# Performance work log

Hardware: AMD Instinct MI355X
Metric: run time of the kernel (lower is better)

## Reference

```python
import jax, jax.numpy as jnp
import numpy as np
import math

# Model dims (from init_kwargs + mamba_ssm Mamba2 defaults)
D_MODEL = 1024
EXPAND = 2
HEADDIM = 64
D_STATE = 64
D_CONV = 4
NGROUPS = 1
D_INNER = EXPAND * D_MODEL            # 2048
NHEADS = D_INNER // HEADDIM           # 32
CONV_DIM = D_INNER + 2 * NGROUPS * D_STATE   # 2176
D_IN_PROJ = 2 * D_INNER + 2 * NGROUPS * D_STATE + NHEADS  # 4256
BATCH, SEQLEN = 4, 2048
RMS_EPS = 1.1920929e-07   # torch.finfo(float32).eps (nn.RMSNorm eps=None)
GNORM_EPS = 1e-5          # mamba_ssm RMSNormGated eps


def _rmsnorm(x, w, eps):
    return x * jax.lax.rsqrt(jnp.mean(x * x, axis=-1, keepdims=True) + eps) * w


def setup_inputs() -> dict:
    key = jax.random.key(0)
    ks = jax.random.split(key, 8)
    x = jax.random.normal(ks[0], (BATCH, SEQLEN, D_MODEL), jnp.float32)
    # router MLP (Linear(d_model,32) -> SiLU -> Linear(32,3))
    r_w1 = jax.random.normal(ks[1], (32, D_MODEL), jnp.float32) / math.sqrt(D_MODEL)
    r_b1 = jnp.zeros((32,), jnp.float32)
    r_w2 = jax.random.normal(ks[2], (3, 32), jnp.float32) / math.sqrt(32)
    r_b2 = jnp.zeros((3,), jnp.float32)
    # Mamba2 params
    in_proj_w = jax.random.normal(ks[3], (D_IN_PROJ, D_MODEL), jnp.float32) / math.sqrt(D_MODEL)
    conv_w = jax.random.normal(ks[4], (CONV_DIM, D_CONV), jnp.float32) * 0.2
    conv_b = jnp.zeros((CONV_DIM,), jnp.float32)
    dt_bias = jax.random.normal(ks[5], (NHEADS,), jnp.float32) * 0.1
    # OrthoSSM multi-scale override: A_log[i] = log(0.001 * 2**i)
    A_log = jnp.log(0.001 * (2.0 ** jnp.arange(NHEADS, dtype=jnp.float32)))
    D_param = jnp.ones((NHEADS,), jnp.float32)
    gnorm_w = jnp.ones((D_INNER,), jnp.float32)
    out_proj_w = jax.random.normal(ks[6], (D_MODEL, D_INNER), jnp.float32) / math.sqrt(D_INNER)
    norm_w = jnp.ones((D_MODEL,), jnp.float32)
    return {"x": x, "norm_w": norm_w, "r_w1": r_w1, "r_b1": r_b1, "r_w2": r_w2,
            "r_b2": r_b2, "in_proj_w": in_proj_w, "conv_w": conv_w, "conv_b": conv_b,
            "dt_bias": dt_bias, "A_log": A_log, "D_param": D_param,
            "gnorm_w": gnorm_w, "out_proj_w": out_proj_w}


def _forward(x, norm_w, r_w1, r_b1, r_w2, r_b2, in_proj_w, conv_w, conv_b,
             dt_bias, A_log, D_param, gnorm_w, out_proj_w):
    B, S, Dm = x.shape
    x_norm = _rmsnorm(x, norm_w, RMS_EPS)
    # --- router: mean-pool -> tiny MLP -> softmax over 3 tiers ---
    h = jax.nn.silu(x_norm.mean(axis=1) @ r_w1.T + r_b1)
    probs = jax.nn.softmax(h @ r_w2.T + r_b2, axis=-1)   # [B,3]
    p_fast = probs[:, 0][:, None, None]
    p_mamba = (probs[:, 1] + probs[:, 2])[:, None, None]
    # --- Mamba2(x_norm) ---
    zxbcdt = x_norm @ in_proj_w.T                         # [B,S,4256]
    z, xBC, dt = jnp.split(zxbcdt, [D_INNER, D_INNER + CONV_DIM], axis=-1)
    # causal depthwise conv1d (kernel 4) + SiLU
    conv = jax.lax.conv_general_dilated(
        xBC.transpose(0, 2, 1), conv_w[:, None, :], (1,), [(D_CONV - 1, 0)],
        feature_group_count=CONV_DIM)                      # [B,CONV_DIM,S]
    xBC = jax.nn.silu(conv.transpose(0, 2, 1) + conv_b)    # [B,S,CONV_DIM]
    xh, Bmat, Cmat = jnp.split(xBC, [D_INNER, D_INNER + NGROUPS * D_STATE], axis=-1)
    xh = xh.reshape(B, S, NHEADS, HEADDIM)                 # [B,S,H,P]
    dt = jax.nn.softplus(dt + dt_bias)                     # [B,S,H]
    A = -jnp.exp(A_log)                                    # [H]
    dA = jnp.exp(dt * A)                                   # [B,S,H]

    def step(hstate, inp):
        dA_t, dt_t, x_t, B_t, C_t = inp
        # hstate: [B,H,P,N]
        hstate = hstate * dA_t[..., None, None] \
                 + (dt_t[..., None] * x_t)[..., None] * B_t[:, None, None, :]
        y_t = jnp.einsum('bhpn,bn->bhp', hstate, C_t)
        return hstate, y_t

    h0 = jnp.zeros((B, NHEADS, HEADDIM, D_STATE), x.dtype)
    xs = (dA.transpose(1, 0, 2), dt.transpose(1, 0, 2), xh.transpose(1, 0, 2, 3),
          Bmat.transpose(1, 0, 2), Cmat.transpose(1, 0, 2))
    _, ys = jax.lax.scan(step, h0, xs)                     # [S,B,H,P]
    y = ys.transpose(1, 0, 2, 3) + D_param[:, None] * xh   # D skip connection
    y = y.reshape(B, S, D_INNER)
    # gated RMSNorm: norm(y * silu(z)) * weight
    yg = y * jax.nn.silu(z)
    yg = _rmsnorm(yg, gnorm_w, GNORM_EPS)
    mamba_out = yg @ out_proj_w.T                          # [B,S,D]
    out = p_fast * x_norm + p_mamba * mamba_out
    return x + out


def reference(x, norm_w, r_w1, r_b1, r_w2, r_b2, in_proj_w, conv_w, conv_b,
              dt_bias, A_log, D_param, gnorm_w, out_proj_w):
    return _forward(x, norm_w, r_w1, r_b1, r_w2, r_b2, in_proj_w, conv_w, conv_b,
                    dt_bias, A_log, D_param, gnorm_w, out_proj_w)
```

## Files before the change

kernel.cpp:

```cpp
#include <hip/hip_runtime.h>
#include <math.h>

typedef __bf16 bf16;
typedef __bf16 bf16x8 __attribute__((ext_vector_type(8)));
typedef __bf16 bf16x4 __attribute__((ext_vector_type(4)));
typedef float f32x4 __attribute__((ext_vector_type(4)));

#define DEV static __device__ __forceinline__
#define AS1 __attribute__((address_space(1)))
#define AS3 __attribute__((address_space(3)))

constexpr int kBatch = 4, kSeq = 2048, kDModel = 1024;
constexpr int kDInner = 2048, kHeads = 32;
constexpr int kConvDim = 2176, kDInProj = 4256, kNPad1 = 4352;
constexpr int kRows = kBatch * kSeq;
constexpr int kChunk = 64, kNChunk = kSeq / kChunk;
constexpr float kRmsEps = 1.1920929e-07f;
constexpr float kGnEps = 1e-5f;

DEV float siluf(float x) { return x / (1.f + expf(-x)); }

DEV float block_reduce_sum(float v, float* red, int tid) {
#pragma unroll
  for (int m = 1; m < 64; m <<= 1) v += __shfl_xor(v, m);
  if ((tid & 63) == 0) red[tid >> 6] = v;
  __syncthreads();
  return red[0] + red[1] + red[2] + red[3];
}

__global__ __launch_bounds__(256) void k_rmsnorm(const float* __restrict__ x,
                                                 const float* __restrict__ nw,
                                                 bf16* __restrict__ xnb) {
  const int row = blockIdx.x;
  const int tid = threadIdx.x;
  float4 v = ((const float4*)(x + (size_t)row * kDModel))[tid];
  __shared__ float red[4];
  float ss = block_reduce_sum(v.x * v.x + v.y * v.y + v.z * v.z + v.w * v.w, red, tid);
  float scale = rsqrtf(ss * (1.f / kDModel) + kRmsEps);
  float4 wv = ((const float4*)nw)[tid];
  bf16x4 ov;
  ov[0] = (bf16)(v.x * scale * wv.x);
  ov[1] = (bf16)(v.y * scale * wv.y);
  ov[2] = (bf16)(v.z * scale * wv.z);
  ov[3] = (bf16)(v.w * scale * wv.w);
  *(bf16x4*)(xnb + (size_t)row * kDModel + tid * 4) = ov;
}

__global__ __launch_bounds__(128) void k_pool1(const bf16* __restrict__ xnb,
                                               float* __restrict__ part) {
  const int g = blockIdx.x, b = blockIdx.y;
  const int tid = threadIdx.x;
  const bf16* base = xnb + ((size_t)b * kSeq + (size_t)g * 32) * kDModel + tid * 8;
  float acc[8] = {0, 0, 0, 0, 0, 0, 0, 0};
  for (int r = 0; r < 32; ++r) {
    bf16x8 v = *(const bf16x8*)(base + (size_t)r * kDModel);
#pragma unroll
    for (int j = 0; j < 8; ++j) acc[j] += (float)v[j];
  }
  float* o = part + ((size_t)b * 64 + g) * kDModel + tid * 8;
#pragma unroll
  for (int j = 0; j < 8; ++j) o[j] = acc[j];
}

__global__ __launch_bounds__(256) void k_pool2(const float* __restrict__ part,
                                               float* __restrict__ mean) {
  const int idx = blockIdx.x * 256 + threadIdx.x;
  const int b = idx >> 10, d = idx & 1023;
  float s = 0.f;
  for (int g = 0; g < 64; ++g) s += part[((size_t)b * 64 + g) * kDModel + d];
  mean[idx] = s * (1.f / kSeq);
}

__global__ __launch_bounds__(128) void k_router(const float* __restrict__ mean,
                                                const float* __restrict__ w1,
                                                const float* __restrict__ b1,
                                                const float* __restrict__ w2,
                                                const float* __restrict__ b2,
                                                float* __restrict__ pfm) {
  __shared__ float hbuf[4][32];
  __shared__ float logit[4][3];
  const int t = threadIdx.x;
  {
    int b = t >> 5, j = t & 31;
    float s = b1[j];
    for (int d = 0; d < kDModel; ++d) s += mean[b * kDModel + d] * w1[j * kDModel + d];
    hbuf[b][j] = siluf(s);
  }
  __syncthreads();
  if (t < 12) {
    int b = t / 3, k = t % 3;
    float s = b2[k];
    for (int j = 0; j < 32; ++j) s += hbuf[b][j] * w2[k * 32 + j];
    logit[b][k] = s;
  }
  __syncthreads();
  if (t < 4) {
    float m = fmaxf(logit[t][0], fmaxf(logit[t][1], logit[t][2]));
    float e0 = expf(logit[t][0] - m), e1 = expf(logit[t][1] - m), e2 = expf(logit[t][2] - m);
    float inv = 1.f / (e0 + e1 + e2);
    pfm[t] = e0 * inv;
    pfm[4 + t] = (e1 + e2) * inv;
  }
}

__global__ __launch_bounds__(256) void k_castpad_w1(const float* __restrict__ w,
                                                    bf16* __restrict__ wb) {
  const size_t idx = (size_t)blockIdx.x * 256 + threadIdx.x;
  const int row = (int)(idx >> 10);
  wb[idx] = (bf16)(row < kDInProj ? w[idx] : 0.f);
}

__global__ __launch_bounds__(256) void k_cast_w2(const float* __restrict__ w,
                                                 bf16* __restrict__ wb) {
  const size_t i4 = (size_t)blockIdx.x * 256 + threadIdx.x;
  float4 v = ((const float4*)w)[i4];
  bf16x4 o;
  o[0] = (bf16)v.x; o[1] = (bf16)v.y; o[2] = (bf16)v.z; o[3] = (bf16)v.w;
  ((bf16x4*)wb)[i4] = o;
}

template <int MF>
__global__ __launch_bounds__(512, 2) void k_gemm(
    const bf16* __restrict__ A, const bf16* __restrict__ B,
    bf16* __restrict__ Cb, float* __restrict__ Cf,
    int K, int Nreal, int ldc, int ntn, int outBf16) {
  constexpr int BM = MF * 32;
  constexpr int GM = MF / 4;
  __shared__ __align__(16) bf16 Al[2][BM][64];
  __shared__ __align__(16) bf16 Bl[2][256][64];
  const int tid = threadIdx.x;
  const int lane = tid & 63, wid = tid >> 6;
  const int wr = wid >> 2, wc = wid & 3;
  const int lr = lane & 15, kb = lane >> 4;
  const int cpx = (int)gridDim.x >> 3;
  const int bid = ((int)blockIdx.x & 7) * cpx + ((int)blockIdx.x >> 3);
  const long n0 = (long)(bid % ntn) * 256;
  const long m0 = (long)(bid / ntn) * BM;

  f32x4 acc[MF][4];
#pragma unroll
  for (int i = 0; i < MF; ++i)
#pragma unroll
    for (int j = 0; j < 4; ++j) acc[i][j] = (f32x4){0.f, 0.f, 0.f, 0.f};

  const int nkt = K >> 6;

#define STAGE(pp, kt)                                                          \
  {                                                                            \
    const long koff = (long)(kt)*64;                                           \
    _Pragma("unroll") for (int j = 0; j < BM / 64; ++j) {                      \
      int idx = j * 512 + tid;                                                 \
      int row = idx >> 3, ch = idx & 7;                                        \
      int cs = ch ^ (row & 7);                                                 \
      __builtin_amdgcn_global_load_lds(                                        \
          (const AS1 void*)(A + (m0 + row) * K + koff + cs * 8),               \
          (AS3 void*)((char*)&Al[pp][0][0] + idx * 16), 16, 0, 0);             \
    }                                                                          \
    _Pragma("unroll") for (int j = 0; j < 4; ++j) {                            \
      int idx = j * 512 + tid;                                                 \
      int row = idx >> 3, ch = idx & 7;                                        \
      int cs = ch ^ (row & 7);                                                 \
      __builtin_amdgcn_global_load_lds(                                        \
          (const AS1 void*)(B + (n0 + row) * K + koff + cs * 8),               \
          (AS3 void*)((char*)&Bl[pp][0][0] + idx * 16), 16, 0, 0);             \
    }                                                                          \
  }
#define RDA(pp, rrow, ks)                                                      \
  (*(const bf16x8*)((const char*)&Al[(pp)][0][0] + (rrow)*128 +                \
                    ((((ks)*4 + kb) ^ (lr & 7)) * 16)))
#define RDB(pp, rrow, ks)                                                      \
  (*(const bf16x8*)((const char*)&Bl[(pp)][0][0] + (rrow)*128 +                \
                    ((((ks)*4 + kb) ^ (lr & 7)) * 16)))

  bf16x8 bfr[4][2];
  bf16x8 afr[2][GM][2];

  STAGE(0, 0);
  __syncthreads();
#pragma unroll
  for (int nf = 0; nf < 4; ++nf)
#pragma unroll
    for (int ks = 0; ks < 2; ++ks) bfr[nf][ks] = RDB(0, wc * 64 + nf * 16 + lr, ks);
#pragma unroll
  for (int g = 0; g < GM; ++g)
#pragma unroll
    for (int ks = 0; ks < 2; ++ks) afr[0][g][ks] = RDA(0, wr * (MF * 16) + g * 16 + lr, ks);

  for (int t = 0; t < nkt; ++t) {
    const int p = t & 1;
    if (t + 1 < nkt) STAGE(p ^ 1, t + 1);
#pragma unroll
    for (int q = 0; q < 4; ++q) {
      if (q < 3) {
#pragma unroll
        for (int g = 0; g < GM; ++g)
#pragma unroll
          for (int ks = 0; ks < 2; ++ks)
            afr[(q + 1) & 1][g][ks] =
                RDA(p, wr * (MF * 16) + ((q + 1) * GM + g) * 16 + lr, ks);
      }
      __builtin_amdgcn_s_setprio(1);
#pragma unroll
      for (int g = 0; g < GM; ++g)
#pragma unroll
        for (int nf = 0; nf < 4; ++nf)
#pragma unroll
          for (int ks = 0; ks < 2; ++ks)
            acc[q * GM + g][nf] = __builtin_amdgcn_mfma_f32_16x16x32_bf16(
                afr[q & 1][g][ks], bfr[nf][ks], acc[q * GM + g][nf], 0, 0, 0);
      __builtin_amdgcn_s_setprio(0);
    }
    if (t + 1 < nkt) {
      __syncthreads();
#pragma unroll
      for (int nf = 0; nf < 4; ++nf)
#pragma unroll
        for (int ks = 0; ks < 2; ++ks)
          bfr[nf][ks] = RDB(p ^ 1, wc * 64 + nf * 16 + lr, ks);
#pragma unroll
      for (int g = 0; g < GM; ++g)
#pragma unroll
        for (int ks = 0; ks < 2; ++ks)
          afr[0][g][ks] = RDA(p ^ 1, wr * (MF * 16) + g * 16 + lr, ks);
    }
  }
#undef STAGE
#undef RDA
#undef RDB

  const int rr = kb * 4;
#pragma unroll
  for (int mf = 0; mf < MF; ++mf) {
#pragma unroll
    for (int nf = 0; nf < 4; ++nf) {
      int col = (int)n0 + wc * 64 + nf * 16 + lr;
      if (col < Nreal) {
        long rbase = m0 + wr * (MF * 16) + mf * 16 + rr;
#pragma unroll
        for (int j = 0; j < 4; ++j) {
          float v = acc[mf][nf][j];
          if (outBf16) Cb[(rbase + j) * (long)ldc + col] = (bf16)v;
          else Cf[(rbase + j) * (long)ldc + col] = v;
        }
      }
    }
  }
}

__global__ __launch_bounds__(256) void k_conv(const bf16* __restrict__ zx,
                                              const float* __restrict__ cw,
                                              const float* __restrict__ cb,
                                              bf16* __restrict__ xbc) {
  const int gid = blockIdx.x * 256 + threadIdx.x;
  if (gid >= kRows * 272) return;
  const int row = gid / 272;
  const int cg = gid - row * 272;
  const int c0 = cg * 8;
  const int s = row & (kSeq - 1);
  const bf16* base = zx + (size_t)row * kDInProj + kDInner + c0;
  bf16x8 z8 = {};
  bf16x8 r3 = *(const bf16x8*)(base);
  bf16x8 r2 = (s >= 1) ? *(const bf16x8*)(base - kDInProj) : z8;
  bf16x8 r1 = (s >= 2) ? *(const bf16x8*)(base - 2 * kDInProj) : z8;
  bf16x8 r0 = (s >= 3) ? *(const bf16x8*)(base - 3 * kDInProj) : z8;
  bf16x8 o;
#pragma unroll
  for (int e = 0; e < 8; ++e) {
    float4 w = ((const float4*)cw)[c0 + e];
    float a = cb[c0 + e] + w.x * (float)r0[e] + w.y * (float)r1[e] +
              w.z * (float)r2[e] + w.w * (float)r3[e];
    o[e] = (bf16)siluf(a);
  }
  *(bf16x8*)(xbc + (size_t)row * kConvDim + c0) = o;
}

__global__ __launch_bounds__(256) void k_dtda(const bf16* __restrict__ zx,
                                              const float* __restrict__ dt_bias,
                                              const float* __restrict__ A_log,
                                              float* __restrict__ dt, float* __restrict__ ldA) {
  const int idx = blockIdx.x * 256 + threadIdx.x;
  const int row = idx >> 5, hh = idx & 31;
  float raw = (float)zx[(size_t)row * kDInProj + (kDInner + kConvDim) + hh] + dt_bias[hh];
  float dtv = (raw > 20.f) ? raw : log1pf(expf(raw));
  dt[idx] = dtv;
  ldA[idx] = dtv * -expf(A_log[hh]);
}

__global__ __launch_bounds__(256) void k_chunkA(
    const bf16* __restrict__ xbc, const float* __restrict__ dtb,
    const float* __restrict__ ldab, float* __restrict__ cumbuf,
    float* __restrict__ Tc, bf16* __restrict__ yb, bf16* __restrict__ Sbuf) {
  const int c = blockIdx.x, h = blockIdx.y, b = blockIdx.z;
  const int tid = threadIdx.x;
  const int w = tid >> 6, lane = tid & 63, lr = lane & 15, kb = lane >> 4;
  const int rr = kb * 4;
  const int t0 = c * kChunk;
  __shared__ bf16 Bl[64 * 72], Cl[64 * 72], XT[64 * 72], WBT[64 * 72], Ml[64 * 72];
  __shared__ float cum_s[64], dt_s[64], w_s[64];

  {
    int s = tid >> 2, q = tid & 3;
    const bf16* rowp = xbc + ((size_t)b * kSeq + t0 + s) * kConvDim;
    bf16x8 x0 = *(const bf16x8*)(rowp + h * 64 + q * 16);
    bf16x8 x1 = *(const bf16x8*)(rowp + h * 64 + q * 16 + 8);
    bf16x8 b0 = *(const bf16x8*)(rowp + kDInner + q * 16);
    bf16x8 b1 = *(const bf16x8*)(rowp + kDInner + q * 16 + 8);
    bf16x8 c0 = *(const bf16x8*)(rowp + kDInner + 64 + q * 16);
    bf16x8 c1 = *(const bf16x8*)(rowp + kDInner + 64 + q * 16 + 8);
    *(bf16x8*)(Bl + s * 72 + q * 16) = b0;
    *(bf16x8*)(Bl + s * 72 + q * 16 + 8) = b1;
    *(bf16x8*)(Cl + s * 72 + q * 16) = c0;
    *(bf16x8*)(Cl + s * 72 + q * 16 + 8) = c1;
#pragma unroll
    for (int e = 0; e < 8; ++e) XT[(q * 16 + e) * 72 + s] = x0[e];
#pragma unroll
    for (int e = 0; e < 8; ++e) XT[(q * 16 + 8 + e) * 72 + s] = x1[e];
  }
  if (tid < 64) {
    size_t di = ((size_t)b * kSeq + t0 + tid) * kHeads + h;
    float v = ldab[di];
    float dtv = dtb[di];
#pragma unroll
    for (int o = 1; o < 64; o <<= 1) {
      float u = __shfl_up(v, o);
      if (lane >= o) v += u;
    }
    cum_s[tid] = v;
    dt_s[tid] = dtv;
    float tot = __shfl(v, 63);
    w_s[tid] = expf(tot - v) * dtv;
    cumbuf[(((size_t)b * kHeads + h) * kNChunk + c) * 64 + tid] = v;
    if (tid == 63) Tc[(b * kHeads + h) * kNChunk + c] = expf(v);
  }
  __syncthreads();

#pragma unroll
  for (int i = 0; i < 16; ++i) {
    int e = i * 256 + tid;
    int n = e >> 6, s = e & 63;
    WBT[n * 72 + s] = (bf16)((float)Bl[s * 72 + n] * w_s[s]);
  }

  f32x4 g[4];
#pragma unroll
  for (int nt = 0; nt < 4; ++nt) g[nt] = (f32x4){0.f, 0.f, 0.f, 0.f};
#pragma unroll
  for (int kk = 0; kk < 2; ++kk) {
    bf16x8 a = *(const bf16x8*)(Cl + (w * 16 + lr) * 72 + kk * 32 + kb * 8);
#pragma unroll
    for (int nt = 0; nt < 4; ++nt) {
      bf16x8 bb = *(const bf16x8*)(Bl + (nt * 16 + lr) * 72 + kk * 32 + kb * 8);
      g[nt] = __builtin_amdgcn_mfma_f32_16x16x32_bf16(a, bb, g[nt], 0, 0, 0);
    }
  }
#pragma unroll
  for (int nt = 0; nt < 4; ++nt)
#pragma unroll
    for (int j = 0; j < 4; ++j) {
      int tt = w * 16 + rr + j, ss = nt * 16 + lr;
      float m = (ss <= tt) ? g[nt][j] * expf(cum_s[tt] - cum_s[ss]) * dt_s[ss] : 0.f;
      Ml[tt * 72 + ss] = (bf16)m;
    }
  __syncthreads();

  f32x4 y4[4];
#pragma unroll
  for (int pt = 0; pt < 4; ++pt) y4[pt] = (f32x4){0.f, 0.f, 0.f, 0.f};
#pragma unroll
  for (int kk = 0; kk < 2; ++kk) {
    bf16x8 a = *(const bf16x8*)(Ml + (w * 16 + lr) * 72 + kk * 32 + kb * 8);
#pragma unroll
    for (int pt = 0; pt < 4; ++pt) {
      bf16x8 bb = *(const bf16x8*)(XT + (pt * 16 + lr) * 72 + kk * 32 + kb * 8);
      y4[pt] = __builtin_amdgcn_mfma_f32_16x16x32_bf16(a, bb, y4[pt], 0, 0, 0);
    }
  }
#pragma unroll
  for (int pt = 0; pt < 4; ++pt)
#pragma unroll
    for (int j = 0; j < 4; ++j) {
      int tt = w * 16 + rr + j, pp = pt * 16 + lr;
      yb[((size_t)b * kSeq + t0 + tt) * kDInner + h * 64 + pp] = (bf16)y4[pt][j];
    }

  f32x4 s4[4];
#pragma unroll
  for (int nt = 0; nt < 4; ++nt) s4[nt] = (f32x4){0.f, 0.f, 0.f, 0.f};
#pragma unroll
  for (int kk = 0; kk < 2; ++kk) {
    bf16x8 a = *(const bf16x8*)(XT + (w * 16 + lr) * 72 + kk * 32 + kb * 8);
#pragma unroll
    for (int nt = 0; nt < 4; ++nt) {
      bf16x8 bb = *(const bf16x8*)(WBT + (nt * 16 + lr) * 72 + kk * 32 + kb * 8);
      s4[nt] = __builtin_amdgcn_mfma_f32_16x16x32_bf16(a, bb, s4[nt], 0, 0, 0);
    }
  }
  const size_t sbase = (((size_t)b * kHeads + h) * kNChunk + c) * 4096;
#pragma unroll
  for (int nt = 0; nt < 4; ++nt)
#pragma unroll
    for (int j = 0; j < 4; ++j) {
      int pp = w * 16 + rr + j, nn = nt * 16 + lr;
      Sbuf[sbase + pp * 64 + nn] = (bf16)s4[nt][j];
    }
}

__global__ __launch_bounds__(256) void k_chunkB(bf16* __restrict__ S,
                                                const float* __restrict__ Tc) {
  const int gid = blockIdx.x * 256 + threadIdx.x;
  const int bh = gid >> 10;
  const int pn = (gid & 1023) << 2;
  bf16* base = S + (size_t)bh * kNChunk * 4096 + pn;
  const float* tc = Tc + bh * kNChunk;
  float4 hh = {0.f, 0.f, 0.f, 0.f};
  bf16x4 s = *(const bf16x4*)(base);
  for (int c = 0; c < kNChunk; ++c) {
    bf16x4 sn = {};
    if (c + 1 < kNChunk) sn = *(const bf16x4*)(base + (size_t)(c + 1) * 4096);
    float t = tc[c];
    bf16x4 ho;
    ho[0] = (bf16)hh.x; ho[1] = (bf16)hh.y; ho[2] = (bf16)hh.z; ho[3] = (bf16)hh.w;
    *(bf16x4*)(base + (size_t)c * 4096) = ho;
    hh.x = t * hh.x + (float)s[0];
    hh.y = t * hh.y + (float)s[1];
    hh.z = t * hh.z + (float)s[2];
    hh.w = t * hh.w + (float)s[3];
    s = sn;
  }
}

__global__ __launch_bounds__(256) void k_chunkC(
    const bf16* __restrict__ xbc, const float* __restrict__ cumbuf,
    const bf16* __restrict__ hs, const float* __restrict__ Dp,
    bf16* __restrict__ yb) {
  const int c = blockIdx.x, h = blockIdx.y, b = blockIdx.z;
  const int tid = threadIdx.x;
  const int w = tid >> 6, lane = tid & 63, lr = lane & 15, kb = lane >> 4;
  const int rr = kb * 4;
  const int t0 = c * kChunk;
  __shared__ bf16 Cl[64 * 72];
  __shared__ float ecum[64];
  {
    int s = tid >> 2, q = tid & 3;
    const bf16* rowp = xbc + ((size_t)b * kSeq + t0 + s) * kConvDim + kDInner + 64 + q * 16;
    *(bf16x8*)(Cl + s * 72 + q * 16) = *(const bf16x8*)rowp;
    *(bf16x8*)(Cl + s * 72 + q * 16 + 8) = *(const bf16x8*)(rowp + 8);
  }
  if (tid < 64)
    ecum[tid] = expf(cumbuf[(((size_t)b * kHeads + h) * kNChunk + c) * 64 + tid]);
  __syncthreads();

  const bf16* hbase = hs + (((size_t)b * kHeads + h) * kNChunk + c) * 4096;
  f32x4 acc[4];
#pragma unroll
  for (int pt = 0; pt < 4; ++pt) acc[pt] = (f32x4){0.f, 0.f, 0.f, 0.f};
#pragma unroll
  for (int kk = 0; kk < 2; ++kk) {
    bf16x8 a = *(const bf16x8*)(Cl + (w * 16 + lr) * 72 + kk * 32 + kb * 8);
#pragma unroll
    for (int pt = 0; pt < 4; ++pt) {
      bf16x8 bb = *(const bf16x8*)(hbase + (pt * 16 + lr) * 64 + kk * 32 + kb * 8);
      acc[pt] = __builtin_amdgcn_mfma_f32_16x16x32_bf16(a, bb, acc[pt], 0, 0, 0);
    }
  }
  const float Dh = Dp[h];
#pragma unroll
  for (int pt = 0; pt < 4; ++pt)
#pragma unroll
    for (int j = 0; j < 4; ++j) {
      int tt = w * 16 + rr + j, pp = pt * 16 + lr;
      size_t ri = (size_t)b * kSeq + t0 + tt;
      size_t yi = ri * kDInner + h * 64 + pp;
      float xv = (float)xbc[ri * kConvDim + h * 64 + pp];
      yb[yi] = (bf16)((float)yb[yi] + ecum[tt] * acc[pt][j] + Dh * xv);
    }
}

__global__ __launch_bounds__(256) void k_gnorm(const bf16* __restrict__ y,
                                               const bf16* __restrict__ zx,
                                               const float* __restrict__ gw,
                                               bf16* __restrict__ yg) {
  const int row = blockIdx.x;
  const int tid = threadIdx.x;
  const int c0 = tid * 8;
  bf16x8 yv = *(const bf16x8*)(y + (size_t)row * kDInner + c0);
  bf16x8 zv = *(const bf16x8*)(zx + (size_t)row * kDInProj + c0);
  float v[8];
  float ss = 0.f;
#pragma unroll
  for (int j = 0; j < 8; ++j) {
    float val = (float)yv[j] * siluf((float)zv[j]);
    v[j] = val;
    ss += val * val;
  }
  __shared__ float red[4];
  ss = block_reduce_sum(ss, red, tid);
  float scale = rsqrtf(ss * (1.f / kDInner) + kGnEps);
  bf16x8 ov;
#pragma unroll
  for (int j = 0; j < 8; ++j) ov[j] = (bf16)(v[j] * scale * gw[c0 + j]);
  *(bf16x8*)(yg + (size_t)row * kDInner + c0) = ov;
}

__global__ __launch_bounds__(256) void k_combine(const float* __restrict__ x,
                                                 const float* __restrict__ nw,
                                                 const bf16* __restrict__ mo,
                                                 const float* __restrict__ pfm,
                                                 float* __restrict__ out) {
  const int row = blockIdx.x;
  const int tid = threadIdx.x;
  const int b = row >> 11;
  float4 v = ((const float4*)(x + (size_t)row * kDModel))[tid];
  __shared__ float red[4];
  float ss = block_reduce_sum(v.x * v.x + v.y * v.y + v.z * v.z + v.w * v.w, red, tid);
  float scale = rsqrtf(ss * (1.f / kDModel) + kRmsEps);
  float pf = pfm[b], pm = pfm[4 + b];
  float4 wv = ((const float4*)nw)[tid];
  bf16x4 mv = *(const bf16x4*)(mo + (size_t)row * kDModel + tid * 4);
  float4 o;
  o.x = v.x + pf * (v.x * scale * wv.x) + pm * (float)mv[0];
  o.y = v.y + pf * (v.y * scale * wv.y) + pm * (float)mv[1];
  o.z = v.z + pf * (v.z * scale * wv.z) + pm * (float)mv[2];
  o.w = v.w + pf * (v.w * scale * wv.w) + pm * (float)mv[3];
  ((float4*)(out + (size_t)row * kDModel))[tid] = o;
}

extern "C" void kernel_launch(void* const* d_in, const int* in_sizes, int n_in,
                              void* d_out, int out_size, void* d_ws, size_t ws_size,
                              hipStream_t stream) {
  const float* x = (const float*)d_in[0];
  const float* norm_w = (const float*)d_in[1];
  const float* r_w1 = (const float*)d_in[2];
  const float* r_b1 = (const float*)d_in[3];
  const float* r_w2 = (const float*)d_in[4];
  const float* r_b2 = (const float*)d_in[5];
  const float* in_proj_w = (const float*)d_in[6];
  const float* conv_w = (const float*)d_in[7];
  const float* conv_b = (const float*)d_in[8];
  const float* dt_bias = (const float*)d_in[9];
  const float* A_log = (const float*)d_in[10];
  const float* D_param = (const float*)d_in[11];
  const float* gnorm_w = (const float*)d_in[12];
  const float* out_proj_w = (const float*)d_in[13];
  float* out = (float*)d_out;
  char* ws = (char*)d_ws;

  bf16* xnb     = (bf16*)(ws + 0);
  bf16* w1b     = (bf16*)(ws + 16777216);
  bf16* zx      = (bf16*)(ws + 25690112);
  bf16* xbc     = (bf16*)(ws + 95420416);
  float* dtb    = (float*)(ws + 131072000);
  float* ldab   = (float*)(ws + 132120576);
  float* cumbuf = (float*)(ws + 133169152);
  float* Tcb    = (float*)(ws + 134217728);
  bf16* yb      = (bf16*)(ws + 134234112);
  bf16* Sbuf    = (bf16*)(ws + 167788544);
  bf16* yg      = (bf16*)(ws + 167788544);
  bf16* w2b     = (bf16*)(ws + 201342976);
  float* part   = (float*)(ws + 205537280);
  float* meanb  = (float*)(ws + 206585856);
  float* pfm    = (float*)(ws + 206602240);
  bf16* mo      = (bf16*)(ws + 95420416);

  k_rmsnorm<<<kRows, 256, 0, stream>>>(x, norm_w, xnb);
  k_pool1<<<dim3(64, 4), 128, 0, stream>>>(xnb, part);
  k_pool2<<<16, 256, 0, stream>>>(part, meanb);
  k_router<<<1, 128, 0, stream>>>(meanb, r_w1, r_b1, r_w2, r_b2, pfm);
  k_castpad_w1<<<kNPad1 * kDModel / 256, 256, 0, stream>>>(in_proj_w, w1b);
  k_cast_w2<<<kDModel * kDInner / 1024, 256, 0, stream>>>(out_proj_w, w2b);
  k_gemm<8><<<(kRows / 256) * (kNPad1 / 256), 512, 0, stream>>>(
      xnb, w1b, zx, nullptr, kDModel, kDInProj, kDInProj, kNPad1 / 256, 1);
  k_conv<<<kRows * 272 / 256, 256, 0, stream>>>(zx, conv_w, conv_b, xbc);
  k_dtda<<<kRows * kHeads / 256, 256, 0, stream>>>(zx, dt_bias, A_log, dtb, ldab);
  k_chunkA<<<dim3(kNChunk, kHeads, kBatch), 256, 0, stream>>>(
      xbc, dtb, ldab, cumbuf, Tcb, yb, Sbuf);
  k_chunkB<<<512, 256, 0, stream>>>(Sbuf, Tcb);
  k_chunkC<<<dim3(kNChunk, kHeads, kBatch), 256, 0, stream>>>(
      xbc, cumbuf, Sbuf, D_param, yb);
  k_gnorm<<<kRows, 256, 0, stream>>>(yb, zx, gnorm_w, yg);
  k_gemm<4><<<(kRows / 128) * (kDModel / 256), 512, 0, stream>>>(
      yg, w2b, mo, nullptr, kDInner, kDModel, kDModel, kDModel / 256, 1);
  k_combine<<<kRows, 256, 0, stream>>>(x, norm_w, mo, pfm, out);
}
```

Before: 355.9 us.

## Retile GEMMs to smaller blocks with K=32 stages and higher occupancy

The GEMM kernel is parameterised by wave grid and N-fragments. Each K stage drops from 64 to 32, using a new packed two-rows-per-line LDS swizzle, and every wave now computes a 64-row tile. In-proj now uses 128x256 tiles and out-proj uses 128x128 tiles with 256 threads. Launch bounds ask for 4 blocks per CU to hide latency through occupancy, at the cost of less data reuse per block and twice as many barriers per K.

```diff
diff --git a/kernel.cpp b/kernel.cpp
--- a/kernel.cpp
+++ b/kernel.cpp
@@ -119,129 +119,103 @@
   ((bf16x4*)wb)[i4] = o;
 }
 
-template <int MF>
-__global__ __launch_bounds__(512, 2) void k_gemm(
+template <int WM, int WN, int NF>
+__global__ __launch_bounds__(WM * WN * 64, 4) void k_gemm(
     const bf16* __restrict__ A, const bf16* __restrict__ B,
-    bf16* __restrict__ Cb, float* __restrict__ Cf,
-    int K, int Nreal, int ldc, int ntn, int outBf16) {
-  constexpr int BM = MF * 32;
-  constexpr int GM = MF / 4;
-  __shared__ __align__(16) bf16 Al[2][BM][64];
-  __shared__ __align__(16) bf16 Bl[2][256][64];
+    bf16* __restrict__ Cb, int K, int Nreal, int ldc, int ntn) {
+  constexpr int THREADS = WM * WN * 64;
+  constexpr int BM = WM * 64;
+  constexpr int BN = WN * NF * 16;
+  constexpr int NA = (BM * 4) / THREADS;
+  constexpr int NB = (BN * 4) / THREADS;
+  __shared__ __align__(16) bf16 Al[2][BM / 2][64];
+  __shared__ __align__(16) bf16 Bl[2][BN / 2][64];
   const int tid = threadIdx.x;
   const int lane = tid & 63, wid = tid >> 6;
-  const int wr = wid >> 2, wc = wid & 3;
+  const int wr = wid / WN, wc = wid % WN;
   const int lr = lane & 15, kb = lane >> 4;
   const int cpx = (int)gridDim.x >> 3;
   const int bid = ((int)blockIdx.x & 7) * cpx + ((int)blockIdx.x >> 3);
-  const long n0 = (long)(bid % ntn) * 256;
+  const long n0 = (long)(bid % ntn) * BN;
   const long m0 = (long)(bid / ntn) * BM;
 
-  f32x4 acc[MF][4];
-#pragma unroll
-  for (int i = 0; i < MF; ++i)
-#pragma unroll
-    for (int j = 0; j < 4; ++j) acc[i][j] = (f32x4){0.f, 0.f, 0.f, 0.f};
-
-  const int nkt = K >> 6;
+  f32x4 acc[4][NF];
+#pragma unroll
+  for (int i = 0; i < 4; ++i)
+#pragma unroll
+    for (int j = 0; j < NF; ++j) acc[i][j] = (f32x4){0.f, 0.f, 0.f, 0.f};
+
+  const int nkt = K >> 5;
 
 #define STAGE(pp, kt)                                                          \
   {                                                                            \
-    const long koff = (long)(kt)*64;                                           \
-    _Pragma("unroll") for (int j = 0; j < BM / 64; ++j) {                      \
-      int idx = j * 512 + tid;                                                 \
-      int row = idx >> 3, ch = idx & 7;                                        \
-      int cs = ch ^ (row & 7);                                                 \
+    const long koff = (long)(kt)*32;                                           \
+    _Pragma("unroll") for (int j = 0; j < NA; ++j) {                           \
+      int idx = j * THREADS + tid;                                             \
+      int line = idx >> 3, sp = (idx & 7) ^ (line & 7);                        \
+      int row = line * 2 + (sp >> 2), ch = sp & 3;                             \
       __builtin_amdgcn_global_load_lds(                                        \
-          (const AS1 void*)(A + (m0 + row) * K + koff + cs * 8),               \
+          (const AS1 void*)(A + (m0 + row) * K + koff + ch * 8),               \
           (AS3 void*)((char*)&Al[pp][0][0] + idx * 16), 16, 0, 0);             \
     }                                                                          \
-    _Pragma("unroll") for (int j = 0; j < 4; ++j) {                            \
-      int idx = j * 512 + tid;                                                 \
-      int row = idx >> 3, ch = idx & 7;                                        \
-      int cs = ch ^ (row & 7);                                                 \
+    _Pragma("unroll") for (int j = 0; j < NB; ++j) {                           \
+      int idx = j * THREADS + tid;                                             \
+      int line = idx >> 3, sp = (idx & 7) ^ (line & 7);                        \
+      int row = line * 2 + (sp >> 2), ch = sp & 3;                             \
       __builtin_amdgcn_global_load_lds(                                        \
-          (const AS1 void*)(B + (n0 + row) * K + koff + cs * 8),               \
+          (const AS1 void*)(B + (n0 + row) * K + koff + ch * 8),               \
           (AS3 void*)((char*)&Bl[pp][0][0] + idx * 16), 16, 0, 0);             \
     }                                                                          \
   }
-#define RDA(pp, rrow, ks)                                                      \
-  (*(const bf16x8*)((const char*)&Al[(pp)][0][0] + (rrow)*128 +                \
-                    ((((ks)*4 + kb) ^ (lr & 7)) * 16)))
-#define RDB(pp, rrow, ks)                                                      \
-  (*(const bf16x8*)((const char*)&Bl[(pp)][0][0] + (rrow)*128 +                \
-                    ((((ks)*4 + kb) ^ (lr & 7)) * 16)))
-
-  bf16x8 bfr[4][2];
-  bf16x8 afr[2][GM][2];
+#define LOFF(r) (((r) >> 1) * 128 + (((((r)&1) << 2) | kb) ^ (((r) >> 1) & 7)) * 16)
+#define RDA(pp, r) (*(const bf16x8*)((const char*)&Al[pp][0][0] + LOFF(r)))
+#define RDB(pp, r) (*(const bf16x8*)((const char*)&Bl[pp][0][0] + LOFF(r)))
+
+  bf16x8 bfr[NF];
+  bf16x8 af[2];
 
   STAGE(0, 0);
   __syncthreads();
 #pragma unroll
-  for (int nf = 0; nf < 4; ++nf)
-#pragma unroll
-    for (int ks = 0; ks < 2; ++ks) bfr[nf][ks] = RDB(0, wc * 64 + nf * 16 + lr, ks);
-#pragma unroll
-  for (int g = 0; g < GM; ++g)
-#pragma unroll
-    for (int ks = 0; ks < 2; ++ks) afr[0][g][ks] = RDA(0, wr * (MF * 16) + g * 16 + lr, ks);
+  for (int nf = 0; nf < NF; ++nf) bfr[nf] = RDB(0, wc * 64 + nf * 16 + lr);
+  af[0] = RDA(0, wr * 64 + lr);
 
   for (int t = 0; t < nkt; ++t) {
     const int p = t & 1;
     if (t + 1 < nkt) STAGE(p ^ 1, t + 1);
 #pragma unroll
     for (int q = 0; q < 4; ++q) {
-      if (q < 3) {
-#pragma unroll
-        for (int g = 0; g < GM; ++g)
-#pragma unroll
-          for (int ks = 0; ks < 2; ++ks)
-            afr[(q + 1) & 1][g][ks] =
-                RDA(p, wr * (MF * 16) + ((q + 1) * GM + g) * 16 + lr, ks);
-      }
+      if (q < 3) af[(q + 1) & 1] = RDA(p, wr * 64 + (q + 1) * 16 + lr);
       __builtin_amdgcn_s_setprio(1);
 #pragma unroll
-      for (int g = 0; g < GM; ++g)
-#pragma unroll
-        for (int nf = 0; nf < 4; ++nf)
-#pragma unroll
-          for (int ks = 0; ks < 2; ++ks)
-            acc[q * GM + g][nf] = __builtin_amdgcn_mfma_f32_16x16x32_bf16(
-                afr[q & 1][g][ks], bfr[nf][ks], acc[q * GM + g][nf], 0, 0, 0);
+      for (int nf = 0; nf < NF; ++nf)
+        acc[q][nf] = __builtin_amdgcn_mfma_f32_16x16x32_bf16(af[q & 1], bfr[nf],
+                                                             acc[q][nf], 0, 0, 0);
       __builtin_amdgcn_s_setprio(0);
     }
     if (t + 1 < nkt) {
       __syncthreads();
 #pragma unroll
-      for (int nf = 0; nf < 4; ++nf)
-#pragma unroll
-        for (int ks = 0; ks < 2; ++ks)
-          bfr[nf][ks] = RDB(p ^ 1, wc * 64 + nf * 16 + lr, ks);
-#pragma unroll
-      for (int g = 0; g < GM; ++g)
-#pragma unroll
-        for (int ks = 0; ks < 2; ++ks)
-          afr[0][g][ks] = RDA(p ^ 1, wr * (MF * 16) + g * 16 + lr, ks);
+      for (int nf = 0; nf < NF; ++nf) bfr[nf] = RDB(p ^ 1, wc * 64 + nf * 16 + lr);
+      af[0] = RDA(p ^ 1, wr * 64 + lr);
     }
   }
 #undef STAGE
+#undef LOFF
 #undef RDA
 #undef RDB
 
   const int rr = kb * 4;
 #pragma unroll
-  for (int mf = 0; mf < MF; ++mf) {
-#pragma unroll
-    for (int nf = 0; nf < 4; ++nf) {
+  for (int mf = 0; mf < 4; ++mf) {
+#pragma unroll
+    for (int nf = 0; nf < NF; ++nf) {
       int col = (int)n0 + wc * 64 + nf * 16 + lr;
       if (col < Nreal) {
-        long rbase = m0 + wr * (MF * 16) + mf * 16 + rr;
-#pragma unroll
-        for (int j = 0; j < 4; ++j) {
-          float v = acc[mf][nf][j];
-          if (outBf16) Cb[(rbase + j) * (long)ldc + col] = (bf16)v;
-          else Cf[(rbase + j) * (long)ldc + col] = v;
-        }
+        long rbase = m0 + wr * 64 + mf * 16 + rr;
+#pragma unroll
+        for (int j = 0; j < 4; ++j)
+          Cb[(rbase + j) * (long)ldc + col] = (bf16)acc[mf][nf][j];
       }
     }
   }
@@ -568,8 +542,8 @@
   k_router<<<1, 128, 0, stream>>>(meanb, r_w1, r_b1, r_w2, r_b2, pfm);
   k_castpad_w1<<<kNPad1 * kDModel / 256, 256, 0, stream>>>(in_proj_w, w1b);
   k_cast_w2<<<kDModel * kDInner / 1024, 256, 0, stream>>>(out_proj_w, w2b);
-  k_gemm<8><<<(kRows / 256) * (kNPad1 / 256), 512, 0, stream>>>(
-      xnb, w1b, zx, nullptr, kDModel, kDInProj, kDInProj, kNPad1 / 256, 1);
+  k_gemm<2, 4, 4><<<(kRows / 128) * (kNPad1 / 256), 512, 0, stream>>>(
+      xnb, w1b, zx, kDModel, kDInProj, kDInProj, kNPad1 / 256);
   k_conv<<<kRows * 272 / 256, 256, 0, stream>>>(zx, conv_w, conv_b, xbc);
   k_dtda<<<kRows * kHeads / 256, 256, 0, stream>>>(zx, dt_bias, A_log, dtb, ldab);
   k_chunkA<<<dim3(kNChunk, kHeads, kBatch), 256, 0, stream>>>(
@@ -578,7 +552,7 @@
   k_chunkC<<<dim3(kNChunk, kHeads, kBatch), 256, 0, stream>>>(
       xbc, cumbuf, Sbuf, D_param, yb);
   k_gnorm<<<kRows, 256, 0, stream>>>(yb, zx, gnorm_w, yg);
-  k_gemm<4><<<(kRows / 128) * (kDModel / 256), 512, 0, stream>>>(
-      yg, w2b, mo, nullptr, kDInner, kDModel, kDModel, kDModel / 256, 1);
+  k_gemm<2, 2, 4><<<(kRows / 128) * (kDModel / 128), 256, 0, stream>>>(
+      yg, w2b, mo, kDInner, kDModel, kDModel, kDModel / 128);
   k_combine<<<kRows, 256, 0, stream>>>(x, norm_w, mo, pfm, out);
 }
```

Result: no change. 355.5 us (-0.1%).
